# Optimization experiments

Measured on AMD Instinct MI355X. Metric: run time of the kernel, lower is better.

Reference implementation:

```python
import jax, jax.numpy as jnp
import numpy as np

B, S, D, K = 16384, 50, 512, 5  # batch, pred_horizon(=steps), dec_units, components_n
H = S  # time_stamp width equals pred_horizon


def setup_inputs() -> dict:
    key = jax.random.key(0)
    ks = jax.random.split(key, 13)
    sc = 0.05
    f32 = jnp.float32
    return {
        "conditions": jax.random.normal(ks[0], (B, S, 3), f32),
        "state_h": jax.random.normal(ks[1], (B, D), f32),
        "state_c": jax.random.normal(ks[2], (B, D), f32),
        # merger LSTM (input = enc_h[D] ++ cond[3])
        "W_m": jax.random.normal(ks[3], (D + 3, 4 * D), f32) * sc,
        "U_m": jax.random.normal(ks[4], (D, 4 * D), f32) * sc,
        "b_m": jnp.zeros((4 * D,), f32),
        # merger MDN heads packed: [alphas|mus_long|sigmas_long|mus_lat|sigmas_lat|rhos]
        "Wh_m": jax.random.normal(ks[5], (D + H, 6 * K), f32) * sc,
        "bh_m": jnp.zeros((6 * K,), f32),
        # yielder LSTM
        "W_y": jax.random.normal(ks[6], (D + 3, 4 * D), f32) * sc,
        "U_y": jax.random.normal(ks[7], (D, 4 * D), f32) * sc,
        "b_y": jnp.zeros((4 * D,), f32),
        # yielder MDN heads packed: [alphas|mus_long|sigmas_long]
        "Wh_y": jax.random.normal(ks[8], (D + H, 3 * K), f32) * sc,
        "bh_y": jnp.zeros((3 * K,), f32),
    }


def _lstm_step(x, h, c, W, U, b):
    # Keras LSTM gate order: i, f, g(cell), o
    z = x @ W + h @ U + b
    i, f, g, o = jnp.split(z, 4, axis=-1)
    c2 = jax.nn.sigmoid(f) * c + jax.nn.sigmoid(i) * jnp.tanh(g)
    h2 = jax.nn.sigmoid(o) * jnp.tanh(c2)
    return h2, c2


def reference(conditions, state_h, state_c, W_m, U_m, b_m, Wh_m, bh_m,
              W_y, U_y, b_y, Wh_y, bh_y):
    # time_stamp[s] = ones in [:s+1] (lower-triangular)
    time_stamp = jnp.tril(jnp.ones((S, H), conditions.dtype))
    enc_h = state_h  # re-fed every step, [B, D]
    # With teacher_percent=1.0 both merger and yielder step conditions are
    # conditions[:, t, :3] at step t (step 0 also uses t=0).
    conds_t = jnp.transpose(conditions, (1, 0, 2))  # [S, B, 3]

    def step(carry, xs):
        h_m, c_m, h_y, c_y = carry
        cond_t, ts = xs  # [B,3], [H]
        x_in = jnp.concatenate([enc_h, cond_t], axis=-1)  # [B, D+3]
        ts_b = jnp.broadcast_to(ts, (h_m.shape[0], H))
        # merger vehicle
        h_m, c_m = _lstm_step(x_in, h_m, c_m, W_m, U_m, b_m)
        feat_m = jnp.concatenate([h_m, ts_b], axis=-1)  # [B, D+H]
        zm = feat_m @ Wh_m + bh_m
        a, ml, sl, mlt, slt, r = jnp.split(zm, 6, axis=-1)
        pm = jnp.concatenate([jax.nn.softmax(a, axis=-1), ml, jnp.exp(sl),
                              mlt, jnp.exp(slt), jnp.tanh(r)], axis=-1)  # [B,30]
        # yielder vehicle
        h_y, c_y = _lstm_step(x_in, h_y, c_y, W_y, U_y, b_y)
        feat_y = jnp.concatenate([h_y, ts_b], axis=-1)
        zy = feat_y @ Wh_y + bh_y
        ay, mly, sly = jnp.split(zy, 3, axis=-1)
        py = jnp.concatenate([jax.nn.softmax(ay, axis=-1), mly, jnp.exp(sly)], axis=-1)  # [B,15]
        return (h_m, c_m, h_y, c_y), (pm, py)

    carry0 = (state_h, state_c, state_h, state_c)
    _, (param_m, param_y) = jax.lax.scan(step, carry0, (conds_t, time_stamp))
    param_m = jnp.transpose(param_m, (1, 0, 2))  # [B, S, 30]
    param_y = jnp.transpose(param_y, (1, 0, 2))  # [B, S, 15]
    return param_m, param_y
```

## Files before the change

### kernel.cpp

```cpp
#include <hip/hip_runtime.h>

typedef __bf16 bf16;
typedef __attribute__((ext_vector_type(8))) __bf16 bf16x8;
typedef __attribute__((ext_vector_type(4))) __bf16 bf16x4;
typedef __attribute__((ext_vector_type(4))) float f32x4;

#define B_TOT 16384
#define SEQ 50
#define DH 512
#define ZW 2048
#define NT 8

#define MFMA16(a, b, c) __builtin_amdgcn_mfma_f32_16x16x32_bf16(a, b, c, 0, 0, 0)

__device__ __forceinline__ float fsigm(float x) {
    return __fdividef(1.0f, 1.0f + __expf(-x));
}
__device__ __forceinline__ float ftanh(float x) {
    float e = __expf(2.0f * x);
    return 1.0f - __fdividef(2.0f, e + 1.0f);
}

__device__ __forceinline__ void gload16(const bf16* g, void* l) {
    __builtin_amdgcn_global_load_lds(
        (const __attribute__((address_space(1))) unsigned int*)g,
        (__attribute__((address_space(3))) unsigned int*)l, 16, 0, 0);
}


__global__ void init_state(const float* __restrict__ sh, const float* __restrict__ sc,
                           bf16* __restrict__ h0m, bf16* __restrict__ h0y,
                           float* __restrict__ cm, float* __restrict__ cy) {
    size_t i = (size_t)blockIdx.x * 256 + threadIdx.x;
    float v = sh[i];
    bf16 hb = (bf16)v;
    h0m[i] = hb;
    h0y[i] = hb;
    float c = sc[i];
    cm[i] = c;
    cy[i] = c;
}

__device__ __forceinline__ int orig_col(int colp) {
    return ((colp >> 4) & 3) * 512 + ((colp >> 6) << 4) + (colp & 15);
}

__global__ void reorder_weights(const float* __restrict__ Um, const float* __restrict__ Uy,
                                const float* __restrict__ Wm, const float* __restrict__ Wy,
                                bf16* __restrict__ UtM, bf16* __restrict__ UtY,
                                bf16* __restrict__ WtM, bf16* __restrict__ WtY) {
    int idx = blockIdx.x * 256 + threadIdx.x;
    int which = idx >> 20;
    int r = idx & ((1 << 20) - 1);
    int colp = r >> 9, k = r & 511;
    int orig = orig_col(colp);
    const float* src = which == 0 ? Um : which == 1 ? Uy : which == 2 ? Wm : Wy;
    bf16* dst = which == 0 ? UtM : which == 1 ? UtY : which == 2 ? WtM : WtY;
    dst[(size_t)colp * 512 + k] = (bf16)src[(size_t)k * ZW + orig];
}

__global__ void build_wc2(const float* __restrict__ Wm, const float* __restrict__ Wy,
                          float* __restrict__ Wc2M, float* __restrict__ Wc2Y) {
    int idx = blockIdx.x * 256 + threadIdx.x;
    if (idx >= 2 * 512 * 12) return;
    int which = idx / 6144;
    int r2 = idx % 6144;
    int hcol = r2 / 12, rg = r2 % 12;
    int r = rg >> 2, g = rg & 3;
    const float* src = which ? Wy : Wm;
    float* dst = which ? Wc2Y : Wc2M;
    dst[hcol * 12 + rg] = src[(size_t)(512 + r) * ZW + g * 512 + hcol];
}

__global__ void cond_transpose(const float* __restrict__ cond, float* __restrict__ condT4) {
    int idx = blockIdx.x * 256 + threadIdx.x;
    if (idx >= SEQ * B_TOT) return;
    int t = idx / B_TOT, row = idx % B_TOT;
    const float* s = cond + ((size_t)row * SEQ + t) * 3;
    f32x4 v = {s[0], s[1], s[2], 0.f};
    *(f32x4*)(condT4 + (size_t)idx * 4) = v;
}

__global__ void build_heads(const float* __restrict__ Whm, const float* __restrict__ bhm,
                            const float* __restrict__ Why, const float* __restrict__ bhy,
                            bf16* __restrict__ WhmT, bf16* __restrict__ WhyT,
                            float* __restrict__ tscm, float* __restrict__ tscy) {
    int i = blockIdx.x * 256 + threadIdx.x;
    const int N1 = 32 * 512, N2 = 16 * 512, N3 = SEQ * 32, N4 = SEQ * 16;
    if (i < N1) {
        int n = i >> 9, k = i & 511;
        WhmT[i] = (bf16)(n < 30 ? Whm[k * 30 + n] : 0.f);
    } else if (i < N1 + N2) {
        int j = i - N1;
        int n = j >> 9, k = j & 511;
        WhyT[j] = (bf16)(n < 15 ? Why[k * 15 + n] : 0.f);
    } else if (i < N1 + N2 + N3) {
        int j = i - (N1 + N2);
        int tt = j >> 5, col = j & 31;
        float v = 0.f;
        if (col < 30) {
            v = bhm[col];
            for (int s = 0; s <= tt; ++s) v += Whm[(512 + s) * 30 + col];
        }
        tscm[j] = v;
    } else if (i < N1 + N2 + N3 + N4) {
        int j = i - (N1 + N2 + N3);
        int tt = j >> 4, col = j & 15;
        float v = 0.f;
        if (col < 15) {
            v = bhy[col];
            for (int s = 0; s <= tt; ++s) v += Why[(512 + s) * 15 + col];
        }
        tscy[j] = v;
    }
}


#define FENCE() asm volatile("" ::: "memory")
#define BARRIER()                        \
    do {                                 \
        FENCE();                         \
        __builtin_amdgcn_s_barrier();    \
        FENCE();                         \
    } while (0)
#define WAIT_LGKM0()                                          \
    do {                                                      \
        asm volatile("s_waitcnt lgkmcnt(0)" ::: "memory");    \
        __builtin_amdgcn_sched_barrier(0);                    \
    } while (0)
#define WAIT_VM4() asm volatile("s_waitcnt vmcnt(4)" ::: "memory")

template <int MODE>
__global__ __launch_bounds__(256, 2) void gemm_step(
    const bf16* __restrict__ Am, const bf16* __restrict__ Ay,
    const bf16* __restrict__ BtM, const bf16* __restrict__ BtY,
    const bf16* __restrict__ xwM, const bf16* __restrict__ xwY,
    const float* __restrict__ Wc2M, const float* __restrict__ Wc2Y,
    const float* __restrict__ biasM, const float* __restrict__ biasY,
    float* __restrict__ cM, float* __restrict__ cY,
    bf16* __restrict__ hoM, bf16* __restrict__ hoY,
    bf16* __restrict__ xoM, bf16* __restrict__ xoY,
    const float* __restrict__ condT4, int t) {
    __shared__ bf16 As[2][2][128][32];
    __shared__ bf16 Bs[2][2][128][32];

    const int tid = threadIdx.x;
    const int wave = tid >> 6, lane = tid & 63;
    const int brow = blockIdx.x * 128, ncb = blockIdx.y * 128;
    const int bz = blockIdx.z;

    const bf16* A = bz ? Ay : Am;
    const bf16* Bt = bz ? BtY : BtM;

    const int fr = lane & 15, fq = lane >> 4;
    const int wr = wave >> 1, wc = wave & 1;

    const int srow = tid >> 2;
    const int sc8 = (((tid & 3) ^ ((srow >> 1) & 3)) << 3);
    const bf16* Asrc = A + (size_t)(brow + srow) * DH + sc8;
    const bf16* Bsrc = Bt + (size_t)(ncb + srow) * DH + sc8;
    char* AsStage = (char*)As + wave * 1024;
    char* BsStage = (char*)Bs + wave * 1024;

    const int cxor = ((fq ^ ((fr >> 1) & 3)) << 4);
    const char* Ard = (char*)As + (wr * 64 + fr) * 64 + cxor;
    const char* Brd = (char*)Bs + (wc * 64 + fr) * 64 + cxor;

    f32x4 acc[4][4];
#pragma unroll
    for (int m = 0; m < 4; ++m)
#pragma unroll
        for (int n = 0; n < 4; ++n) acc[m][n] = (f32x4){0.f, 0.f, 0.f, 0.f};

    bf16x8 af[4], bg[4];

#define STAGE_A(pb, kh, kts)                                  \
    do {                                                      \
        const bf16* _s = Asrc + (kts) * 64 + (kh) * 32;       \
        char* _d = AsStage + (pb) * 16384 + (kh) * 8192;      \
        gload16(_s, _d);                                      \
        gload16(_s + 64 * DH, _d + 4096);                     \
    } while (0)
#define STAGE_B(pb, kh, kts)                                  \
    do {                                                      \
        const bf16* _s = Bsrc + (kts) * 64 + (kh) * 32;       \
        char* _d = BsStage + (pb) * 16384 + (kh) * 8192;      \
        gload16(_s, _d);                                      \
        gload16(_s + 64 * DH, _d + 4096);                     \
    } while (0)
#define LOAD_AF(pb, kh)                                                   \
    do {                                                                  \
        const char* _a = Ard + (pb) * 16384 + (kh) * 8192;                \
        af[0] = *(const bf16x8*)(_a);                                     \
        af[1] = *(const bf16x8*)(_a + 1024);                              \
        af[2] = *(const bf16x8*)(_a + 2048);                              \
        af[3] = *(const bf16x8*)(_a + 3072);                              \
    } while (0)
#define LOAD_BG(pb, kh)                                                   \
    do {                                                                  \
        const char* _b = Brd + (pb) * 16384 + (kh) * 8192;                \
        bg[0] = *(const bf16x8*)(_b);                                     \
        bg[1] = *(const bf16x8*)(_b + 1024);                              \
        bg[2] = *(const bf16x8*)(_b + 2048);                              \
        bg[3] = *(const bf16x8*)(_b + 3072);                              \
    } while (0)
#define MFMA_Q()                                                          \
    do {                                                                  \
        __builtin_amdgcn_s_setprio(1);                                    \
        _Pragma("unroll") for (int _m = 0; _m < 4; ++_m)                  \
            _Pragma("unroll") for (int _n = 0; _n < 4; ++_n)              \
                acc[_m][_n] = MFMA16(af[_m], bg[_n], acc[_m][_n]);        \
        __builtin_amdgcn_s_setprio(0);                                    \
        __builtin_amdgcn_sched_barrier(0);                                \
    } while (0)

    STAGE_A(0, 0, 0);
    STAGE_B(0, 0, 0);
    STAGE_A(0, 1, 0);
    STAGE_B(0, 1, 0);
    STAGE_A(1, 0, 1);
    STAGE_B(1, 0, 1);
    WAIT_VM4();
    BARRIER();

    for (int kt = 0; kt < NT; ++kt) {
        const int p = kt & 1, q = p ^ 1;
        const int t1 = (kt + 1 < NT) ? kt + 1 : NT - 1;
        const int t2 = (kt + 2 < NT) ? kt + 2 : NT - 1;
        LOAD_AF(p, 0);
        LOAD_BG(p, 0);
        STAGE_A(q, 1, t1);
        STAGE_B(q, 1, t1);
        BARRIER();
        WAIT_LGKM0();
        MFMA_Q();
        WAIT_VM4();
        BARRIER();
        LOAD_AF(p, 1);
        LOAD_BG(p, 1);
        STAGE_A(p, 0, t2);
        STAGE_B(p, 0, t2);
        BARRIER();
        WAIT_LGKM0();
        MFMA_Q();
        WAIT_VM4();
        BARRIER();
    }

    const int jb = blockIdx.y * 2 + wc;
    const int hcol = jb * 16 + fr;
    const int rowbase = brow + wr * 64 + fq * 4;

    if (MODE == 0) {
        const float* bias = bz ? biasY : biasM;
        bf16* XO = bz ? xoY : xoM;
#pragma unroll
        for (int m = 0; m < 4; ++m)
#pragma unroll
            for (int j = 0; j < 4; ++j) {
                const int row = rowbase + m * 16 + j;
                bf16x4 v;
#pragma unroll
                for (int n = 0; n < 4; ++n) v[n] = (bf16)(acc[m][n][j] + bias[n * 512 + hcol]);
                *(bf16x4*)(XO + (size_t)row * ZW + hcol * 4) = v;
            }
    } else {
        float* Cb = bz ? cY : cM;
        bf16* Ho = bz ? hoY : hoM;
        const bf16* xw = bz ? xwY : xwM;
        const float* Wc2 = bz ? Wc2Y : Wc2M;
        f32x4 wcv0 = *(const f32x4*)(Wc2 + hcol * 12);
        f32x4 wcv1 = *(const f32x4*)(Wc2 + hcol * 12 + 4);
        f32x4 wcv2 = *(const f32x4*)(Wc2 + hcol * 12 + 8);
        bf16x4 xwv[4][4];
        float cv[4][4];
#pragma unroll
        for (int m = 0; m < 4; ++m)
#pragma unroll
            for (int j = 0; j < 4; ++j) {
                const int row = rowbase + m * 16 + j;
                xwv[m][j] = *(const bf16x4*)(xw + (size_t)row * ZW + hcol * 4);
                cv[m][j] = Cb[(size_t)row * DH + hcol];
            }
#pragma unroll
        for (int m = 0; m < 4; ++m) {
            f32x4 cd[4];
#pragma unroll
            for (int j = 0; j < 4; ++j)
                cd[j] = *(const f32x4*)(condT4 + ((size_t)t * B_TOT + rowbase + m * 16 + j) * 4);
#pragma unroll
            for (int j = 0; j < 4; ++j) {
                float z[4];
#pragma unroll
                for (int g = 0; g < 4; ++g)
                    z[g] = acc[m][g][j] + (float)xwv[m][j][g] + cd[j][0] * wcv0[g] +
                           cd[j][1] * wcv1[g] + cd[j][2] * wcv2[g];
                float ii = fsigm(z[0]);
                float ff = fsigm(z[1]);
                float gg = ftanh(z[2]);
                float oo = fsigm(z[3]);
                const int row = rowbase + m * 16 + j;
                size_t ci = (size_t)row * DH + hcol;
                float cn = ff * cv[m][j] + ii * gg;
                Cb[ci] = cn;
                Ho[ci] = (bf16)(oo * ftanh(cn));
            }
        }
    }
#undef STAGE_A
#undef STAGE_B
#undef LOAD_AF
#undef LOAD_BG
#undef MFMA_Q
}

__global__ __launch_bounds__(128) void heads_step(
    const bf16* __restrict__ hm, const bf16* __restrict__ hy,
    const bf16* __restrict__ WhmT, const bf16* __restrict__ WhyT,
    const float* __restrict__ tscm, const float* __restrict__ tscy,
    float* __restrict__ out, int t) {
    __shared__ float zbuf[2 * 768];
    const int tid = threadIdx.x, wave = tid >> 6, lane = tid & 63;
    const int fr = lane & 15, fq = lane >> 4;
    const int rbase = blockIdx.x * 32 + wave * 16;

    f32x4 am0 = {0.f, 0.f, 0.f, 0.f}, am1 = {0.f, 0.f, 0.f, 0.f}, ay0 = {0.f, 0.f, 0.f, 0.f};

    for (int k0 = 0; k0 < DH; k0 += 32) {
        const size_t ao = (size_t)(rbase + fr) * DH + k0 + fq * 8;
        bf16x8 a0 = *(const bf16x8*)(hm + ao);
        bf16x8 y0 = *(const bf16x8*)(hy + ao);
        const size_t bo = (size_t)fr * DH + k0 + fq * 8;
        bf16x8 b0 = *(const bf16x8*)(WhmT + bo);
        bf16x8 b1 = *(const bf16x8*)(WhmT + bo + 16 * DH);
        bf16x8 yb = *(const bf16x8*)(WhyT + bo);
        am0 = MFMA16(a0, b0, am0);
        am1 = MFMA16(a0, b1, am1);
        ay0 = MFMA16(y0, yb, ay0);
    }

    float* zm = zbuf + wave * 768;
    float* zy = zm + 512;
#pragma unroll
    for (int j = 0; j < 4; ++j) {
        int rl = fq * 4 + j;
        zm[rl * 32 + fr] = am0[j] + tscm[t * 32 + fr];
        zm[rl * 32 + 16 + fr] = am1[j] + tscm[t * 32 + 16 + fr];
        zy[rl * 16 + fr] = ay0[j] + tscy[t * 16 + fr];
    }
    __syncthreads();

    const int r = lane & 15;
    const size_t grow = (size_t)rbase + r;
    if (lane < 16) {
        float z[30];
#pragma unroll
        for (int i = 0; i < 30; ++i) z[i] = zm[r * 32 + i];
        float* o = out + (grow * SEQ + t) * 30;
        float mx = z[0];
#pragma unroll
        for (int i = 1; i < 5; ++i) mx = fmaxf(mx, z[i]);
        float e[5], s = 0.f;
#pragma unroll
        for (int i = 0; i < 5; ++i) {
            e[i] = __expf(z[i] - mx);
            s += e[i];
        }
        float inv = __fdividef(1.f, s);
#pragma unroll
        for (int i = 0; i < 5; ++i) o[i] = e[i] * inv;
#pragma unroll
        for (int i = 5; i < 10; ++i) o[i] = z[i];
#pragma unroll
        for (int i = 10; i < 15; ++i) o[i] = __expf(z[i]);
#pragma unroll
        for (int i = 15; i < 20; ++i) o[i] = z[i];
#pragma unroll
        for (int i = 20; i < 25; ++i) o[i] = __expf(z[i]);
#pragma unroll
        for (int i = 25; i < 30; ++i) o[i] = ftanh(z[i]);
    } else if (lane < 32) {
        float z[15];
#pragma unroll
        for (int i = 0; i < 15; ++i) z[i] = zy[r * 16 + i];
        float* o = out + (size_t)B_TOT * SEQ * 30 + (grow * SEQ + t) * 15;
        float mx = z[0];
#pragma unroll
        for (int i = 1; i < 5; ++i) mx = fmaxf(mx, z[i]);
        float e[5], s = 0.f;
#pragma unroll
        for (int i = 0; i < 5; ++i) {
            e[i] = __expf(z[i] - mx);
            s += e[i];
        }
        float inv = __fdividef(1.f, s);
#pragma unroll
        for (int i = 0; i < 5; ++i) o[i] = e[i] * inv;
#pragma unroll
        for (int i = 5; i < 10; ++i) o[i] = z[i];
#pragma unroll
        for (int i = 10; i < 15; ++i) o[i] = __expf(z[i]);
    }
}

extern "C" void kernel_launch(void* const* d_in, const int* in_sizes, int n_in,
                              void* d_out, int out_size, void* d_ws, size_t ws_size,
                              hipStream_t stream) {
    const float* cond = (const float*)d_in[0];
    const float* sh = (const float*)d_in[1];
    const float* sc = (const float*)d_in[2];
    const float* Wm = (const float*)d_in[3];
    const float* Um = (const float*)d_in[4];
    const float* bm = (const float*)d_in[5];
    const float* Whm = (const float*)d_in[6];
    const float* bhm = (const float*)d_in[7];
    const float* Wy = (const float*)d_in[8];
    const float* Uy = (const float*)d_in[9];
    const float* by_ = (const float*)d_in[10];
    const float* Why = (const float*)d_in[11];
    const float* bhy = (const float*)d_in[12];
    float* out = (float*)d_out;

    char* p = (char*)d_ws;
    auto take = [&](size_t bytes) {
        char* r = p;
        p += (bytes + 255) & ~(size_t)255;
        return r;
    };
    bf16* UtM = (bf16*)take((size_t)ZW * DH * 2);
    bf16* UtY = (bf16*)take((size_t)ZW * DH * 2);
    bf16* WtM = (bf16*)take((size_t)ZW * DH * 2);
    bf16* WtY = (bf16*)take((size_t)ZW * DH * 2);
    float* Wc2M = (float*)take(512 * 12 * 4);
    float* Wc2Y = (float*)take(512 * 12 * 4);
    bf16* WhmT = (bf16*)take(32 * DH * 2);
    bf16* WhyT = (bf16*)take(16 * DH * 2);
    float* tscm = (float*)take(SEQ * 32 * 4);
    float* tscy = (float*)take(SEQ * 16 * 4);
    float* condT4 = (float*)take((size_t)SEQ * B_TOT * 4 * 4);
    bf16* xwM = (bf16*)take((size_t)B_TOT * ZW * 2);
    bf16* xwY = (bf16*)take((size_t)B_TOT * ZW * 2);
    bf16* hM0 = (bf16*)take((size_t)B_TOT * DH * 2);
    bf16* hM1 = (bf16*)take((size_t)B_TOT * DH * 2);
    bf16* hY0 = (bf16*)take((size_t)B_TOT * DH * 2);
    bf16* hY1 = (bf16*)take((size_t)B_TOT * DH * 2);
    float* cMb = (float*)take((size_t)B_TOT * DH * 4);
    float* cYb = (float*)take((size_t)B_TOT * DH * 4);
    bf16* hM[2] = {hM0, hM1};
    bf16* hY[2] = {hY0, hY1};

    init_state<<<(B_TOT * DH) / 256, 256, 0, stream>>>(sh, sc, hM0, hY0, cMb, cYb);
    reorder_weights<<<(4 * ZW * DH) / 256, 256, 0, stream>>>(Um, Uy, Wm, Wy, UtM, UtY, WtM, WtY);
    build_wc2<<<(2 * 512 * 12 + 255) / 256, 256, 0, stream>>>(Wm, Wy, Wc2M, Wc2Y);
    cond_transpose<<<(SEQ * B_TOT + 255) / 256, 256, 0, stream>>>(cond, condT4);
    build_heads<<<(32 * 512 + 16 * 512 + SEQ * 32 + SEQ * 16 + 255) / 256, 256, 0, stream>>>(
        Whm, bhm, Why, bhy, WhmT, WhyT, tscm, tscy);

    dim3 ggrid(B_TOT / 128, ZW / 128, 2);
    gemm_step<0><<<ggrid, 256, 0, stream>>>(hM0, hM0, WtM, WtY, nullptr, nullptr,
                                            nullptr, nullptr, bm, by_, nullptr, nullptr,
                                            nullptr, nullptr, xwM, xwY, condT4, 0);

    for (int t = 0; t < SEQ; ++t) {
        const int a = t & 1, b = (t + 1) & 1;
        gemm_step<1><<<ggrid, 256, 0, stream>>>(hM[a], hY[a], UtM, UtY, xwM, xwY,
                                                Wc2M, Wc2Y, nullptr, nullptr, cMb, cYb,
                                                hM[b], hY[b], nullptr, nullptr, condT4, t);
        heads_step<<<B_TOT / 32, 128, 0, stream>>>(hM[b], hY[b], WhmT, WhyT, tscm, tscy, out, t);
    }
}
```

Baseline: 8.019 ms.

## Fold heads into next step's GEMM grid and use triple-buffered k-loop

Previous step's MDN heads computation runs as extra blocks (z=2) inside the recurrent GEMM launch instead of a separate kernel per step, with a final standalone heads launch for the last step. The GEMM main loop is restructured from a double-buffered, two-half-tile scheme into a 3-stage ring of 32-wide k-tiles with one barrier per iteration, and launch bounds raised to 3 blocks per CU. This removes 49 kernel launches and lets the heads overlap with the GEMM, at the cost of register pressure from the higher occupancy target and extra grid blocks (many of which exit immediately).

After: 8.478 ms. +5.7%, slower.

```diff
diff --git a/kernel.cpp b/kernel.cpp
--- a/kernel.cpp
+++ b/kernel.cpp
@@ -9,7 +9,7 @@
 #define SEQ 50
 #define DH 512
 #define ZW 2048
-#define NT 8
+#define NT 16
 
 #define MFMA16(a, b, c) __builtin_amdgcn_mfma_f32_16x16x32_bf16(a, b, c, 0, 0, 0)
 
@@ -129,9 +129,10 @@
         __builtin_amdgcn_sched_barrier(0);                    \
     } while (0)
 #define WAIT_VM4() asm volatile("s_waitcnt vmcnt(4)" ::: "memory")
+#define WAIT_VM0() asm volatile("s_waitcnt vmcnt(0)" ::: "memory")
 
 template <int MODE>
-__global__ __launch_bounds__(256, 2) void gemm_step(
+__global__ __launch_bounds__(256, 3) void gemm_step(
     const bf16* __restrict__ Am, const bf16* __restrict__ Ay,
     const bf16* __restrict__ BtM, const bf16* __restrict__ BtY,
     const bf16* __restrict__ xwM, const bf16* __restrict__ xwY,
@@ -140,31 +141,120 @@
     float* __restrict__ cM, float* __restrict__ cY,
     bf16* __restrict__ hoM, bf16* __restrict__ hoY,
     bf16* __restrict__ xoM, bf16* __restrict__ xoY,
-    const float* __restrict__ condT4, int t) {
-    __shared__ bf16 As[2][2][128][32];
-    __shared__ bf16 Bs[2][2][128][32];
+    const float* __restrict__ condT4,
+    const bf16* __restrict__ WhmT, const bf16* __restrict__ WhyT,
+    const float* __restrict__ tscm, const float* __restrict__ tscy,
+    float* __restrict__ out, int t) {
+    __shared__ __align__(16) char smem[49152];
 
     const int tid = threadIdx.x;
     const int wave = tid >> 6, lane = tid & 63;
+    const int bz = blockIdx.z;
+    const int fr = lane & 15, fq = lane >> 4;
+
+    if (MODE == 1 && bz == 2) {
+        if (t == 0) return;
+        const int hb = blockIdx.y * 128 + blockIdx.x;
+        if (hb >= 256) return;
+        const int th = t - 1;
+        const int rbase = hb * 64 + wave * 16;
+
+        f32x4 am0 = {0.f, 0.f, 0.f, 0.f}, am1 = {0.f, 0.f, 0.f, 0.f},
+              ay0 = {0.f, 0.f, 0.f, 0.f};
+        for (int k0 = 0; k0 < DH; k0 += 32) {
+            const size_t ao = (size_t)(rbase + fr) * DH + k0 + fq * 8;
+            bf16x8 a0 = *(const bf16x8*)(Am + ao);
+            bf16x8 y0 = *(const bf16x8*)(Ay + ao);
+            const size_t bo = (size_t)fr * DH + k0 + fq * 8;
+            bf16x8 b0 = *(const bf16x8*)(WhmT + bo);
+            bf16x8 b1 = *(const bf16x8*)(WhmT + bo + 16 * DH);
+            bf16x8 yb = *(const bf16x8*)(WhyT + bo);
+            am0 = MFMA16(a0, b0, am0);
+            am1 = MFMA16(a0, b1, am1);
+            ay0 = MFMA16(y0, yb, ay0);
+        }
+
+        float* zm = (float*)smem + wave * 768;
+        float* zy = zm + 512;
+#pragma unroll
+        for (int j = 0; j < 4; ++j) {
+            int rl = fq * 4 + j;
+            zm[rl * 32 + fr] = am0[j] + tscm[th * 32 + fr];
+            zm[rl * 32 + 16 + fr] = am1[j] + tscm[th * 32 + 16 + fr];
+            zy[rl * 16 + fr] = ay0[j] + tscy[th * 16 + fr];
+        }
+        __syncthreads();
+
+        const int r = lane & 15;
+        const size_t grow = (size_t)rbase + r;
+        if (lane < 16) {
+            float z[30];
+#pragma unroll
+            for (int i = 0; i < 30; ++i) z[i] = zm[r * 32 + i];
+            float* o = out + (grow * SEQ + th) * 30;
+            float mx = z[0];
+#pragma unroll
+            for (int i = 1; i < 5; ++i) mx = fmaxf(mx, z[i]);
+            float e[5], s = 0.f;
+#pragma unroll
+            for (int i = 0; i < 5; ++i) {
+                e[i] = __expf(z[i] - mx);
+                s += e[i];
+            }
+            float inv = __fdividef(1.f, s);
+#pragma unroll
+            for (int i = 0; i < 5; ++i) o[i] = e[i] * inv;
+#pragma unroll
+            for (int i = 5; i < 10; ++i) o[i] = z[i];
+#pragma unroll
+            for (int i = 10; i < 15; ++i) o[i] = __expf(z[i]);
+#pragma unroll
+            for (int i = 15; i < 20; ++i) o[i] = z[i];
+#pragma unroll
+            for (int i = 20; i < 25; ++i) o[i] = __expf(z[i]);
+#pragma unroll
+            for (int i = 25; i < 30; ++i) o[i] = ftanh(z[i]);
+        } else if (lane < 32) {
+            float z[15];
+#pragma unroll
+            for (int i = 0; i < 15; ++i) z[i] = zy[r * 16 + i];
+            float* o = out + (size_t)B_TOT * SEQ * 30 + (grow * SEQ + th) * 15;
+            float mx = z[0];
+#pragma unroll
+            for (int i = 1; i < 5; ++i) mx = fmaxf(mx, z[i]);
+            float e[5], s = 0.f;
+#pragma unroll
+            for (int i = 0; i < 5; ++i) {
+                e[i] = __expf(z[i] - mx);
+                s += e[i];
+            }
+            float inv = __fdividef(1.f, s);
+#pragma unroll
+            for (int i = 0; i < 5; ++i) o[i] = e[i] * inv;
+#pragma unroll
+            for (int i = 5; i < 10; ++i) o[i] = z[i];
+#pragma unroll
+            for (int i = 10; i < 15; ++i) o[i] = __expf(z[i]);
+        }
+        return;
+    }
+
     const int brow = blockIdx.x * 128, ncb = blockIdx.y * 128;
-    const int bz = blockIdx.z;
-
     const bf16* A = bz ? Ay : Am;
     const bf16* Bt = bz ? BtY : BtM;
 
-    const int fr = lane & 15, fq = lane >> 4;
     const int wr = wave >> 1, wc = wave & 1;
 
     const int srow = tid >> 2;
     const int sc8 = (((tid & 3) ^ ((srow >> 1) & 3)) << 3);
     const bf16* Asrc = A + (size_t)(brow + srow) * DH + sc8;
     const bf16* Bsrc = Bt + (size_t)(ncb + srow) * DH + sc8;
-    char* AsStage = (char*)As + wave * 1024;
-    char* BsStage = (char*)Bs + wave * 1024;
+    char* stA = smem + wave * 1024;
+    char* stB = smem + 8192 + wave * 1024;
 
     const int cxor = ((fq ^ ((fr >> 1) & 3)) << 4);
-    const char* Ard = (char*)As + (wr * 64 + fr) * 64 + cxor;
-    const char* Brd = (char*)Bs + (wc * 64 + fr) * 64 + cxor;
+    const char* Ard = smem + (wr * 64 + fr) * 64 + cxor;
+    const char* Brd = smem + 8192 + (wc * 64 + fr) * 64 + cxor;
 
     f32x4 acc[4][4];
 #pragma unroll
@@ -174,77 +264,52 @@
 
     bf16x8 af[4], bg[4];
 
-#define STAGE_A(pb, kh, kts)                                  \
-    do {                                                      \
-        const bf16* _s = Asrc + (kts) * 64 + (kh) * 32;       \
-        char* _d = AsStage + (pb) * 16384 + (kh) * 8192;      \
-        gload16(_s, _d);                                      \
-        gload16(_s + 64 * DH, _d + 4096);                     \
+#define STAGE_T(buf, kts)                                   \
+    do {                                                    \
+        const bf16* _sa = Asrc + (kts) * 32;                \
+        const bf16* _sb = Bsrc + (kts) * 32;                \
+        char* _da = stA + (buf) * 16384;                    \
+        char* _db = stB + (buf) * 16384;                    \
+        gload16(_sa, _da);                                  \
+        gload16(_sa + 64 * DH, _da + 4096);                 \
+        gload16(_sb, _db);                                  \
+        gload16(_sb + 64 * DH, _db + 4096);                 \
     } while (0)
-#define STAGE_B(pb, kh, kts)                                  \
-    do {                                                      \
-        const bf16* _s = Bsrc + (kts) * 64 + (kh) * 32;       \
-        char* _d = BsStage + (pb) * 16384 + (kh) * 8192;      \
-        gload16(_s, _d);                                      \
-        gload16(_s + 64 * DH, _d + 4096);                     \
-    } while (0)
-#define LOAD_AF(pb, kh)                                                   \
-    do {                                                                  \
-        const char* _a = Ard + (pb) * 16384 + (kh) * 8192;                \
-        af[0] = *(const bf16x8*)(_a);                                     \
-        af[1] = *(const bf16x8*)(_a + 1024);                              \
-        af[2] = *(const bf16x8*)(_a + 2048);                              \
-        af[3] = *(const bf16x8*)(_a + 3072);                              \
-    } while (0)
-#define LOAD_BG(pb, kh)                                                   \
-    do {                                                                  \
-        const char* _b = Brd + (pb) * 16384 + (kh) * 8192;                \
-        bg[0] = *(const bf16x8*)(_b);                                     \
-        bg[1] = *(const bf16x8*)(_b + 1024);                              \
-        bg[2] = *(const bf16x8*)(_b + 2048);                              \
-        bg[3] = *(const bf16x8*)(_b + 3072);                              \
-    } while (0)
-#define MFMA_Q()                                                          \
-    do {                                                                  \
-        __builtin_amdgcn_s_setprio(1);                                    \
-        _Pragma("unroll") for (int _m = 0; _m < 4; ++_m)                  \
-            _Pragma("unroll") for (int _n = 0; _n < 4; ++_n)              \
-                acc[_m][_n] = MFMA16(af[_m], bg[_n], acc[_m][_n]);        \
-        __builtin_amdgcn_s_setprio(0);                                    \
-        __builtin_amdgcn_sched_barrier(0);                                \
-    } while (0)
-
-    STAGE_A(0, 0, 0);
-    STAGE_B(0, 0, 0);
-    STAGE_A(0, 1, 0);
-    STAGE_B(0, 1, 0);
-    STAGE_A(1, 0, 1);
-    STAGE_B(1, 0, 1);
+
+    STAGE_T(0, 0);
+    STAGE_T(1, 1);
     WAIT_VM4();
-    BARRIER();
-
+
+#pragma unroll
     for (int kt = 0; kt < NT; ++kt) {
-        const int p = kt & 1, q = p ^ 1;
-        const int t1 = (kt + 1 < NT) ? kt + 1 : NT - 1;
-        const int t2 = (kt + 2 < NT) ? kt + 2 : NT - 1;
-        LOAD_AF(p, 0);
-        LOAD_BG(p, 0);
-        STAGE_A(q, 1, t1);
-        STAGE_B(q, 1, t1);
+        const int p = kt % 3;
         BARRIER();
+        if (kt + 2 < NT) STAGE_T((kt + 2) % 3, kt + 2);
+        {
+            const char* _a = Ard + p * 16384;
+            af[0] = *(const bf16x8*)(_a);
+            af[1] = *(const bf16x8*)(_a + 1024);
+            af[2] = *(const bf16x8*)(_a + 2048);
+            af[3] = *(const bf16x8*)(_a + 3072);
+            const char* _b = Brd + p * 16384;
+            bg[0] = *(const bf16x8*)(_b);
+            bg[1] = *(const bf16x8*)(_b + 1024);
+            bg[2] = *(const bf16x8*)(_b + 2048);
+            bg[3] = *(const bf16x8*)(_b + 3072);
+        }
         WAIT_LGKM0();
-        MFMA_Q();
-        WAIT_VM4();
-        BARRIER();
-        LOAD_AF(p, 1);
-        LOAD_BG(p, 1);
-        STAGE_A(p, 0, t2);
-        STAGE_B(p, 0, t2);
-        BARRIER();
-        WAIT_LGKM0();
-        MFMA_Q();
-        WAIT_VM4();
-        BARRIER();
+        __builtin_amdgcn_s_setprio(1);
+#pragma unroll
+        for (int m = 0; m < 4; ++m)
+#pragma unroll
+            for (int n = 0; n < 4; ++n) acc[m][n] = MFMA16(af[m], bg[n], acc[m][n]);
+        __builtin_amdgcn_s_setprio(0);
+        __builtin_amdgcn_sched_barrier(0);
+        if (kt == NT - 2) {
+            WAIT_VM0();
+        } else {
+            WAIT_VM4();
+        }
     }
 
     const int jb = blockIdx.y * 2 + wc;
@@ -307,11 +372,7 @@
             }
         }
     }
-#undef STAGE_A
-#undef STAGE_B
-#undef LOAD_AF
-#undef LOAD_BG
-#undef MFMA_Q
+#undef STAGE_T
 }
 
 __global__ __launch_bounds__(128) void heads_step(
@@ -456,16 +517,20 @@
     build_heads<<<(32 * 512 + 16 * 512 + SEQ * 32 + SEQ * 16 + 255) / 256, 256, 0, stream>>>(
         Whm, bhm, Why, bhy, WhmT, WhyT, tscm, tscy);
 
-    dim3 ggrid(B_TOT / 128, ZW / 128, 2);
-    gemm_step<0><<<ggrid, 256, 0, stream>>>(hM0, hM0, WtM, WtY, nullptr, nullptr,
-                                            nullptr, nullptr, bm, by_, nullptr, nullptr,
-                                            nullptr, nullptr, xwM, xwY, condT4, 0);
-
+    dim3 ggrid0(B_TOT / 128, ZW / 128, 2);
+    gemm_step<0><<<ggrid0, 256, 0, stream>>>(hM0, hM0, WtM, WtY, nullptr, nullptr,
+                                             nullptr, nullptr, bm, by_, nullptr, nullptr,
+                                             nullptr, nullptr, xwM, xwY, condT4,
+                                             nullptr, nullptr, nullptr, nullptr, nullptr, 0);
+
+    dim3 ggrid1(B_TOT / 128, ZW / 128, 3);
     for (int t = 0; t < SEQ; ++t) {
         const int a = t & 1, b = (t + 1) & 1;
-        gemm_step<1><<<ggrid, 256, 0, stream>>>(hM[a], hY[a], UtM, UtY, xwM, xwY,
-                                                Wc2M, Wc2Y, nullptr, nullptr, cMb, cYb,
-                                                hM[b], hY[b], nullptr, nullptr, condT4, t);
-        heads_step<<<B_TOT / 32, 128, 0, stream>>>(hM[b], hY[b], WhmT, WhyT, tscm, tscy, out, t);
-    }
-}
+        gemm_step<1><<<ggrid1, 256, 0, stream>>>(hM[a], hY[a], UtM, UtY, xwM, xwY,
+                                                 Wc2M, Wc2Y, nullptr, nullptr, cMb, cYb,
+                                                 hM[b], hY[b], nullptr, nullptr, condT4,
+                                                 WhmT, WhyT, tscm, tscy, out, t);
+    }
+    heads_step<<<B_TOT / 32, 128, 0, stream>>>(hM[SEQ & 1], hY[SEQ & 1], WhmT, WhyT,
+                                               tscm, tscy, out, SEQ - 1);
+}
```

## Load recurrent weights directly into registers in MFMA fragment layout, triple-buffer A

Applied to the files above, without the earlier changes.

Reorders the U/W weight matrices into a per-lane MFMA fragment layout so each wave can fetch its B operands straight from global memory into registers, with no LDS staging. Only the activation tile goes through LDS, now in a three-slot ring with a 32-wide K step and one barrier per iteration instead of four. The smaller LDS footprint permits three blocks per CU via launch bounds. The cost is more global traffic per wave for B (no sharing through LDS) and more register pressure from the double-buffered B fragments.

Result: no change. 7.943 ms (-1.0%).

```diff
diff --git a/kernel.cpp b/kernel.cpp
--- a/kernel.cpp
+++ b/kernel.cpp
@@ -4,12 +4,13 @@
 typedef __attribute__((ext_vector_type(8))) __bf16 bf16x8;
 typedef __attribute__((ext_vector_type(4))) __bf16 bf16x4;
 typedef __attribute__((ext_vector_type(4))) float f32x4;
+typedef __attribute__((ext_vector_type(4))) int i32x4;
 
 #define B_TOT 16384
 #define SEQ 50
 #define DH 512
 #define ZW 2048
-#define NT 8
+#define NT 16
 
 #define MFMA16(a, b, c) __builtin_amdgcn_mfma_f32_16x16x32_bf16(a, b, c, 0, 0, 0)
 
@@ -56,7 +57,10 @@
     int orig = orig_col(colp);
     const float* src = which == 0 ? Um : which == 1 ? Uy : which == 2 ? Wm : Wy;
     bf16* dst = which == 0 ? UtM : which == 1 ? UtY : which == 2 ? WtM : WtY;
-    dst[(size_t)colp * 512 + k] = (bf16)src[(size_t)k * ZW + orig];
+    int cb = colp >> 4, fr = colp & 15;
+    int kt = k >> 5, fq = (k >> 3) & 3, e = k & 7;
+    int lane = fq * 16 + fr;
+    dst[(((size_t)(cb * 16 + kt) * 64 + lane) << 3) + e] = (bf16)src[(size_t)k * ZW + orig];
 }
 
 __global__ void build_wc2(const float* __restrict__ Wm, const float* __restrict__ Wy,
@@ -128,10 +132,14 @@
         asm volatile("s_waitcnt lgkmcnt(0)" ::: "memory");    \
         __builtin_amdgcn_sched_barrier(0);                    \
     } while (0)
-#define WAIT_VM4() asm volatile("s_waitcnt vmcnt(4)" ::: "memory")
+#define WAIT_VM(n)                                                  \
+    do {                                                            \
+        asm volatile("s_waitcnt vmcnt(" #n ")" ::: "memory");       \
+        __builtin_amdgcn_sched_barrier(0);                          \
+    } while (0)
 
 template <int MODE>
-__global__ __launch_bounds__(256, 2) void gemm_step(
+__global__ __launch_bounds__(256, 3) void gemm_step(
     const bf16* __restrict__ Am, const bf16* __restrict__ Ay,
     const bf16* __restrict__ BtM, const bf16* __restrict__ BtY,
     const bf16* __restrict__ xwM, const bf16* __restrict__ xwY,
@@ -141,14 +149,12 @@
     bf16* __restrict__ hoM, bf16* __restrict__ hoY,
     bf16* __restrict__ xoM, bf16* __restrict__ xoY,
     const float* __restrict__ condT4, int t) {
-    __shared__ bf16 As[2][2][128][32];
-    __shared__ bf16 Bs[2][2][128][32];
+    __shared__ bf16 As[3][128][32];
 
     const int tid = threadIdx.x;
     const int wave = tid >> 6, lane = tid & 63;
     const int brow = blockIdx.x * 128, ncb = blockIdx.y * 128;
     const int bz = blockIdx.z;
-
     const bf16* A = bz ? Ay : Am;
     const bf16* Bt = bz ? BtY : BtM;
 
@@ -158,13 +164,13 @@
     const int srow = tid >> 2;
     const int sc8 = (((tid & 3) ^ ((srow >> 1) & 3)) << 3);
     const bf16* Asrc = A + (size_t)(brow + srow) * DH + sc8;
-    const bf16* Bsrc = Bt + (size_t)(ncb + srow) * DH + sc8;
-    char* AsStage = (char*)As + wave * 1024;
-    char* BsStage = (char*)Bs + wave * 1024;
+    char* stA = (char*)As + wave * 1024;
 
     const int cxor = ((fq ^ ((fr >> 1) & 3)) << 4);
     const char* Ard = (char*)As + (wr * 64 + fr) * 64 + cxor;
-    const char* Brd = (char*)Bs + (wc * 64 + fr) * 64 + cxor;
+
+    const uint64_t bbase =
+        (uint64_t)(const char*)Bt + (uint64_t)(blockIdx.y * 8 + wc * 4) * 16384 + lane * 16;
 
     f32x4 acc[4][4];
 #pragma unroll
@@ -172,79 +178,79 @@
 #pragma unroll
         for (int n = 0; n < 4; ++n) acc[m][n] = (f32x4){0.f, 0.f, 0.f, 0.f};
 
-    bf16x8 af[4], bg[4];
-
-#define STAGE_A(pb, kh, kts)                                  \
-    do {                                                      \
-        const bf16* _s = Asrc + (kts) * 64 + (kh) * 32;       \
-        char* _d = AsStage + (pb) * 16384 + (kh) * 8192;      \
-        gload16(_s, _d);                                      \
-        gload16(_s + 64 * DH, _d + 4096);                     \
+    i32x4 bgbuf[2][4];
+
+#define STAGE(slot, kts)                                    \
+    do {                                                    \
+        const bf16* _s = Asrc + (kts) * 32;                 \
+        char* _d = stA + (slot) * 8192;                     \
+        gload16(_s, _d);                                    \
+        gload16(_s + 64 * DH, _d + 4096);                   \
     } while (0)
-#define STAGE_B(pb, kh, kts)                                  \
-    do {                                                      \
-        const bf16* _s = Bsrc + (kts) * 64 + (kh) * 32;       \
-        char* _d = BsStage + (pb) * 16384 + (kh) * 8192;      \
-        gload16(_s, _d);                                      \
-        gload16(_s + 64 * DH, _d + 4096);                     \
+
+#define BGLOAD(bank, kts)                                                        \
+    do {                                                                         \
+        uint64_t _a = bbase + (uint64_t)(kts) * 1024;                            \
+        asm volatile("global_load_dwordx4 %0, %1, off"                          \
+                     : "=&v"(bgbuf[bank][0]) : "v"(_a) : "memory");              \
+        asm volatile("global_load_dwordx4 %0, %1, off"                          \
+                     : "=&v"(bgbuf[bank][1]) : "v"(_a + 16384) : "memory");      \
+        asm volatile("global_load_dwordx4 %0, %1, off"                          \
+                     : "=&v"(bgbuf[bank][2]) : "v"(_a + 32768) : "memory");      \
+        asm volatile("global_load_dwordx4 %0, %1, off"                          \
+                     : "=&v"(bgbuf[bank][3]) : "v"(_a + 49152) : "memory");      \
     } while (0)
-#define LOAD_AF(pb, kh)                                                   \
-    do {                                                                  \
-        const char* _a = Ard + (pb) * 16384 + (kh) * 8192;                \
-        af[0] = *(const bf16x8*)(_a);                                     \
-        af[1] = *(const bf16x8*)(_a + 1024);                              \
-        af[2] = *(const bf16x8*)(_a + 2048);                              \
-        af[3] = *(const bf16x8*)(_a + 3072);                              \
-    } while (0)
-#define LOAD_BG(pb, kh)                                                   \
-    do {                                                                  \
-        const char* _b = Brd + (pb) * 16384 + (kh) * 8192;                \
-        bg[0] = *(const bf16x8*)(_b);                                     \
-        bg[1] = *(const bf16x8*)(_b + 1024);                              \
-        bg[2] = *(const bf16x8*)(_b + 2048);                              \
-        bg[3] = *(const bf16x8*)(_b + 3072);                              \
-    } while (0)
-#define MFMA_Q()                                                          \
-    do {                                                                  \
-        __builtin_amdgcn_s_setprio(1);                                    \
-        _Pragma("unroll") for (int _m = 0; _m < 4; ++_m)                  \
-            _Pragma("unroll") for (int _n = 0; _n < 4; ++_n)              \
-                acc[_m][_n] = MFMA16(af[_m], bg[_n], acc[_m][_n]);        \
-        __builtin_amdgcn_s_setprio(0);                                    \
-        __builtin_amdgcn_sched_barrier(0);                                \
-    } while (0)
-
-    STAGE_A(0, 0, 0);
-    STAGE_B(0, 0, 0);
-    STAGE_A(0, 1, 0);
-    STAGE_B(0, 1, 0);
-    STAGE_A(1, 0, 1);
-    STAGE_B(1, 0, 1);
-    WAIT_VM4();
+
+    BGLOAD(0, 0);
+    STAGE(0, 0);
+    STAGE(1, 1);
+    WAIT_VM(2);
     BARRIER();
 
-    for (int kt = 0; kt < NT; ++kt) {
-        const int p = kt & 1, q = p ^ 1;
-        const int t1 = (kt + 1 < NT) ? kt + 1 : NT - 1;
-        const int t2 = (kt + 2 < NT) ? kt + 2 : NT - 1;
-        LOAD_AF(p, 0);
-        LOAD_BG(p, 0);
-        STAGE_A(q, 1, t1);
-        STAGE_B(q, 1, t1);
+#pragma unroll
+    for (int kt = 0; kt < NT - 1; ++kt) {
+        const int rcur = kt % 3;
+        STAGE((kt + 2) % 3, (kt + 2 < NT) ? kt + 2 : NT - 1);
+        BGLOAD((kt + 1) & 1, kt + 1);
+        bf16x8 af[4];
+        {
+            const char* _a = Ard + rcur * 8192;
+            af[0] = *(const bf16x8*)(_a);
+            af[1] = *(const bf16x8*)(_a + 1024);
+            af[2] = *(const bf16x8*)(_a + 2048);
+            af[3] = *(const bf16x8*)(_a + 3072);
+        }
+        WAIT_LGKM0();
+        WAIT_VM(6);
+        __builtin_amdgcn_s_setprio(1);
+#pragma unroll
+        for (int m = 0; m < 4; ++m)
+#pragma unroll
+            for (int n = 0; n < 4; ++n)
+                acc[m][n] = MFMA16(af[m], __builtin_bit_cast(bf16x8, bgbuf[kt & 1][n]),
+                                   acc[m][n]);
+        __builtin_amdgcn_s_setprio(0);
+        __builtin_amdgcn_sched_barrier(0);
         BARRIER();
+    }
+    {
+        bf16x8 af[4];
+        const char* _a = Ard + ((NT - 1) % 3) * 8192;
+        af[0] = *(const bf16x8*)(_a);
+        af[1] = *(const bf16x8*)(_a + 1024);
+        af[2] = *(const bf16x8*)(_a + 2048);
+        af[3] = *(const bf16x8*)(_a + 3072);
         WAIT_LGKM0();
-        MFMA_Q();
-        WAIT_VM4();
-        BARRIER();
-        LOAD_AF(p, 1);
-        LOAD_BG(p, 1);
-        STAGE_A(p, 0, t2);
-        STAGE_B(p, 0, t2);
-        BARRIER();
-        WAIT_LGKM0();
-        MFMA_Q();
-        WAIT_VM4();
-        BARRIER();
+        WAIT_VM(0);
+        __builtin_amdgcn_s_setprio(1);
+#pragma unroll
+        for (int m = 0; m < 4; ++m)
+#pragma unroll
+            for (int n = 0; n < 4; ++n)
+                acc[m][n] = MFMA16(af[m], __builtin_bit_cast(bf16x8, bgbuf[(NT - 1) & 1][n]),
+                                   acc[m][n]);
+        __builtin_amdgcn_s_setprio(0);
+        __builtin_amdgcn_sched_barrier(0);
     }
 
     const int jb = blockIdx.y * 2 + wc;
@@ -307,11 +313,8 @@
             }
         }
     }
-#undef STAGE_A
-#undef STAGE_B
-#undef LOAD_AF
-#undef LOAD_BG
-#undef MFMA_Q
+#undef STAGE
+#undef BGLOAD
 }
 
 __global__ __launch_bounds__(128) void heads_step(
```
